# Performance work log

Hardware: AMD Instinct MI355X
Metric: run time of the kernel (lower is better)

The kernel has to match this reference:

```python
import jax, jax.numpy as jnp
import numpy as np

B, N, D, E = 128, 512, 256, 8192  # graphs, nodes/graph, embed_dim, edges/graph
K = int(np.ceil(0.8 * N))         # TopKPooling ratio=0.8 -> k per graph


def setup_inputs() -> dict:
    key = jax.random.key(0)
    ks = jax.random.split(key, 16)
    Ntot = B * N
    x = jax.random.normal(ks[0], (Ntot, 4), jnp.float32)
    offs = (jnp.arange(B, dtype=jnp.int32) * N)[:, None]
    src = (jax.random.randint(ks[1], (B, E), 0, N, jnp.int32) + offs).reshape(-1)
    dst = (jax.random.randint(ks[2], (B, E), 0, N, jnp.int32) + offs).reshape(-1)
    s = 0.05
    w = lambda k, shape: jax.random.normal(k, shape, jnp.float32) * s
    return {
        'x': x, 'src': src, 'dst': dst,
        'Wr1': w(ks[3], (4, D)), 'Ws1': w(ks[4], (4, D)), 'b1': jnp.zeros((D,), jnp.float32),
        'Wr2': w(ks[5], (D, D)), 'Ws2': w(ks[6], (D, D)), 'b2': jnp.zeros((D,), jnp.float32),
        'Wr3': w(ks[7], (D, D)), 'Ws3': w(ks[8], (D, D)), 'b3': jnp.zeros((D,), jnp.float32),
        'p_attn': w(ks[9], (D,)),
        'W1': w(ks[10], (2 * D, D)), 'c1': jnp.zeros((D,), jnp.float32),
        'W2': w(ks[11], (D, D // 2)), 'c2': jnp.zeros((D // 2,), jnp.float32),
        'W3': w(ks[12], (D // 2, 1)), 'c3': jnp.zeros((1,), jnp.float32),
    }


def _graph_conv(x, src, dst, Wr, Ws, b):
    # PyG GraphConv, aggr='add': out = lin_rel(sum_{j in N(i)} x_j) + lin_root(x_i)
    agg = jax.ops.segment_sum(x[src], dst, num_segments=B * N)
    return agg @ Wr + b + x @ Ws


def _gmp_gap(xb):
    # xb: [B, n, D] -> concat(global max pool, global mean pool): [B, 2D]
    return jnp.concatenate([xb.max(axis=1), xb.mean(axis=1)], axis=1)


def reference(x, src, dst, Wr1, Ws1, b1, Wr2, Ws2, b2, Wr3, Ws3, b3,
              p_attn, W1, c1, W2, c2, W3, c3):
    h = jax.nn.relu(_graph_conv(x, src, dst, Wr1, Ws1, b1))
    x1 = _gmp_gap(h.reshape(B, N, D))
    h = jax.nn.relu(_graph_conv(h, src, dst, Wr2, Ws2, b2))
    x2 = _gmp_gap(h.reshape(B, N, D))
    h = jax.nn.relu(_graph_conv(h, src, dst, Wr3, Ws3, b3))
    # TopKPooling: score = x.p/||p||; keep top-k per graph; scale by tanh(score)
    score = (h @ p_attn) / (jnp.linalg.norm(p_attn) + 1e-16)
    vals, idx = jax.lax.top_k(score.reshape(B, N), K)           # [B, K]
    hb = h.reshape(B, N, D)
    sel = jnp.take_along_axis(hb, idx[:, :, None], axis=1) * jnp.tanh(vals)[:, :, None]
    x3 = _gmp_gap(sel)
    z = x1 + x2 + x3
    z = jax.nn.relu(z @ W1 + c1)
    z = jax.nn.relu(z @ W2 + c2)  # dropout is identity in eval mode
    return jax.nn.sigmoid(z @ W3 + c3)[:, 0]
```

## Files before the change

kernel.cpp:

```cpp
#include <hip/hip_runtime.h>

typedef unsigned short u16;
typedef unsigned int u32;

#define B_GRAPHS 128
#define N_NODES  512
#define D_DIM    256
#define E_EDGES  8192
#define K_TOP    410
#define CSR_STRIDE 12288
#define AS 132

typedef __attribute__((ext_vector_type(8))) __bf16 bf16x8;
typedef __attribute__((ext_vector_type(4))) float  f32x4;

__device__ __forceinline__ float bf2f(u16 h) {
  union { u32 u; float f; } c; c.u = ((u32)h) << 16; return c.f;
}
__device__ __forceinline__ float u2f(u32 u) {
  union { u32 u; float f; } c; c.u = u; return c.f;
}
__device__ __forceinline__ u16 f2bf(float f) {
  union { float f; u32 u; } c; c.f = f;
  u32 u = c.u;
  u += 0x7fffu + ((u >> 16) & 1u);
  return (u16)(u >> 16);
}
__device__ __forceinline__ void async_copy16(const void* g, void* l) {
  __builtin_amdgcn_global_load_lds((const __attribute__((address_space(1))) void*)g,
                                   (__attribute__((address_space(3))) void*)l, 16, 0, 0);
}

__global__ void zero_kernel(float* __restrict__ p) {
  *(float4*)&p[(size_t)(blockIdx.x * 256 + threadIdx.x) * 4] = float4{0.f, 0.f, 0.f, 0.f};
}

__global__ void prep_kernel(const float* __restrict__ Wr2, const float* __restrict__ Ws2,
                            const float* __restrict__ Wr3, const float* __restrict__ Ws3,
                            u16* __restrict__ WT) {
  const int mat = blockIdx.y;
  const int n = blockIdx.x;
  const int k = threadIdx.x;
  const float* W = (mat == 0) ? Wr2 : (mat == 1) ? Ws2 : (mat == 2) ? Wr3 : Ws3;
  WT[((size_t)mat << 16) + ((size_t)n << 8) + k] = f2bf(W[(size_t)k * 256 + n]);
}

__global__ __launch_bounds__(256) void csr_kernel(const int* __restrict__ src,
                                                  const int* __restrict__ dst,
                                                  u16* __restrict__ csr_col,
                                                  u32* __restrict__ csr_off) {
  __shared__ u32 cnt[512];
  __shared__ u32 poff[513];
  const int g = blockIdx.x, t = threadIdx.x;
  const int base = g * N_NODES, ebase = g * E_EDGES;
  for (int i = t; i < 512; i += 256) cnt[i] = 0;
  __syncthreads();
  for (int e = t; e < E_EDGES; e += 256)
    atomicAdd(&cnt[dst[ebase + e] - base], 1u);
  __syncthreads();
  if (t == 0) {
    u32 run = 0;
    for (int i = 0; i < 512; ++i) { poff[i] = run; run += (cnt[i] + 7u) & ~7u; }
    poff[512] = run;
  }
  __syncthreads();
  for (int i = t; i < 513; i += 256) csr_off[(size_t)g * 513 + i] = poff[i];
  for (int i = t; i < 512; i += 256) {
    const u32 s = poff[i] + cnt[i], e2 = poff[i + 1];
    for (u32 k = s; k < e2; ++k) csr_col[(size_t)g * CSR_STRIDE + k] = 512;
  }
  __syncthreads();
  for (int i = t; i < 512; i += 256) cnt[i] = poff[i];
  __syncthreads();
  for (int e = t; e < E_EDGES; e += 256) {
    const int d = dst[ebase + e] - base;
    const int s = src[ebase + e] - base;
    const u32 pos = atomicAdd(&cnt[d], 1u);
    csr_col[(size_t)g * CSR_STRIDE + pos] = (u16)s;
  }
}

__global__ __launch_bounds__(256) void conv1_kernel(const float* __restrict__ x,
                             const u16* __restrict__ csr_col, const u32* __restrict__ csr_off,
                             const float* __restrict__ Wr1, const float* __restrict__ Ws1,
                             const float* __restrict__ b1,
                             u16* __restrict__ H1, float* __restrict__ X1) {
  __shared__ float xs[513 * 4];
  __shared__ float aggs[N_NODES * 5];
  __shared__ __align__(16) u16 cols[CSR_STRIDE];
  __shared__ u32 offs[513];
  const int c = blockIdx.x;
  const int g = blockIdx.y;
  const int base = g * N_NODES;
  const int t = threadIdx.x;

  for (int i = t; i < N_NODES; i += 256)
    *(float4*)&xs[i * 4] = *(const float4*)&x[(size_t)(base + i) * 4];
  if (t < 4) xs[512 * 4 + t] = 0.f;
  for (int i = t; i < CSR_STRIDE / 2; i += 256)
    ((u32*)cols)[i] = ((const u32*)(csr_col + (size_t)g * CSR_STRIDE))[i];
  for (int i = t; i < 513; i += 256) offs[i] = csr_off[(size_t)g * 513 + i];
  __syncthreads();

  #pragma unroll
  for (int nn = 0; nn < 2; ++nn) {
    const int i = t * 2 + nn;
    const u32 s0 = offs[i];
    const int nb = (int)((offs[i + 1] - s0) >> 3);
    float a0 = 0.f, a1 = 0.f, a2 = 0.f, a3 = 0.f;
    for (int b = 0; b < nb; ++b) {
      const uint4 cw = *(const uint4*)&cols[s0 + (u32)b * 8];
      const u32 ww[4] = {cw.x, cw.y, cw.z, cw.w};
      #pragma unroll
      for (int q = 0; q < 4; ++q) {
        const int ca = ww[q] & 0xffffu, cb = ww[q] >> 16;
        const float4 va = *(const float4*)&xs[ca * 4];
        const float4 vb = *(const float4*)&xs[cb * 4];
        a0 += va.x + vb.x; a1 += va.y + vb.y;
        a2 += va.z + vb.z; a3 += va.w + vb.w;
      }
    }
    aggs[i * 5 + 0] = a0; aggs[i * 5 + 1] = a1;
    aggs[i * 5 + 2] = a2; aggs[i * 5 + 3] = a3;
  }
  __syncthreads();

  float wr[4], wsv[4];
  #pragma unroll
  for (int k = 0; k < 4; ++k) { wr[k] = Wr1[k * 256 + t]; wsv[k] = Ws1[k * 256 + t]; }
  const float bb = b1[t];
  float mx = 0.f, sm = 0.f;
  const int nlo = c * 256;
  for (int n = nlo; n < nlo + 256; ++n) {
    float acc = bb;
    #pragma unroll
    for (int k = 0; k < 4; ++k) acc += aggs[n * 5 + k] * wr[k] + xs[n * 4 + k] * wsv[k];
    acc = fmaxf(acc, 0.f);
    H1[(size_t)(base + n) * D_DIM + t] = f2bf(acc);
    mx = fmaxf(mx, acc);
    sm += acc;
  }
  atomicMax((int*)&X1[(size_t)g * 512 + t], __float_as_int(mx));
  atomicAdd(&X1[(size_t)g * 512 + 256 + t], sm);
}

__global__ __launch_bounds__(512) void agg_gather_kernel(const u16* __restrict__ H,
                                                         const u16* __restrict__ csr_col,
                                                         const u32* __restrict__ csr_off,
                                                         u16* __restrict__ AGG) {
  __shared__ __align__(16) u16 hs[513 * AS];
  __shared__ __align__(16) u16 cols[CSR_STRIDE];
  __shared__ u32 offs[513];
  const int c = blockIdx.x;
  const int g = blockIdx.y;
  const int base = g * N_NODES;
  const int t = threadIdx.x;

  #pragma unroll
  for (int p = 0; p < 32; ++p) {
    const int flat = p * 512 + t;
    const int row = flat >> 5, q = flat & 31;
    *(uint2*)&hs[row * AS + q * 4] =
        *(const uint2*)&H[(size_t)(base + row) * D_DIM + c * 128 + q * 4];
  }
  if (t < 33) *(uint2*)&hs[512 * AS + t * 4] = uint2{0u, 0u};
  #pragma unroll
  for (int p = 0; p < 12; ++p)
    ((u32*)cols)[p * 512 + t] = ((const u32*)(csr_col + (size_t)g * CSR_STRIDE))[p * 512 + t];
  for (int i = t; i < 513; i += 512) offs[i] = csr_off[(size_t)g * 513 + i];
  __syncthreads();

  const int w = t >> 6, lane = t & 63;
  const int h2 = lane >> 5, fl = lane & 31;
  const int i0 = w * 64;
  for (int i = i0; i < i0 + 64; ++i) {
    const u32 s0 = offs[i];
    const int nb = (int)((offs[i + 1] - s0) >> 3);
    float a0 = 0.f, a1 = 0.f, a2 = 0.f, a3 = 0.f;
    if (nb > 0) {
      uint4 cw = *(const uint4*)&cols[s0];
      for (int b = 0; b < nb; ++b) {
        uint4 cwn = cw;
        if (b + 1 < nb) cwn = *(const uint4*)&cols[s0 + (u32)(b + 1) * 8];
        const u32 w01 = h2 ? cw.z : cw.x;
        const u32 w23 = h2 ? cw.w : cw.y;
        const int c0 = w01 & 0xffffu, c1 = w01 >> 16;
        const int c2 = w23 & 0xffffu, c3 = w23 >> 16;
        const uint2 d0 = *(const uint2*)&hs[c0 * AS + fl * 4];
        const uint2 d1 = *(const uint2*)&hs[c1 * AS + fl * 4];
        const uint2 d2 = *(const uint2*)&hs[c2 * AS + fl * 4];
        const uint2 d3 = *(const uint2*)&hs[c3 * AS + fl * 4];
        a0 += u2f(d0.x << 16); a1 += u2f(d0.x & 0xffff0000u);
        a2 += u2f(d0.y << 16); a3 += u2f(d0.y & 0xffff0000u);
        a0 += u2f(d1.x << 16); a1 += u2f(d1.x & 0xffff0000u);
        a2 += u2f(d1.y << 16); a3 += u2f(d1.y & 0xffff0000u);
        a0 += u2f(d2.x << 16); a1 += u2f(d2.x & 0xffff0000u);
        a2 += u2f(d2.y << 16); a3 += u2f(d2.y & 0xffff0000u);
        a0 += u2f(d3.x << 16); a1 += u2f(d3.x & 0xffff0000u);
        a2 += u2f(d3.y << 16); a3 += u2f(d3.y & 0xffff0000u);
        cw = cwn;
      }
    }
    a0 += __shfl_xor(a0, 32); a1 += __shfl_xor(a1, 32);
    a2 += __shfl_xor(a2, 32); a3 += __shfl_xor(a3, 32);
    if (h2 == 0) {
      uint2 o;
      o.x = (u32)f2bf(a0) | ((u32)f2bf(a1) << 16);
      o.y = (u32)f2bf(a2) | ((u32)f2bf(a3) << 16);
      *(uint2*)&AGG[(size_t)(base + i) * D_DIM + c * 128 + fl * 4] = o;
    }
  }
}

__global__ __launch_bounds__(256) void gemm_kernel(const u16* __restrict__ Amat,
                                                   const u16* __restrict__ Hmat,
                                                   const u16* __restrict__ WrT,
                                                   const u16* __restrict__ WsT,
                                                   const float* __restrict__ bias,
                                                   u16* __restrict__ Hout,
                                                   float* __restrict__ x2pool,
                                                   float* __restrict__ score,
                                                   const float* __restrict__ pvec) {
  __shared__ __align__(16) u16 At[128 * 32];
  __shared__ __align__(16) u16 Bt[128 * 32];
  const int m0 = blockIdx.x * 128;
  const int n0 = blockIdx.y * 128;
  const int t = threadIdx.x;
  const int wid = t >> 6, lane = t & 63;
  const int wm = wid >> 1, wn = wid & 1;
  const int r16 = lane & 15, q0 = lane >> 4;

  f32x4 acc[4][4];
  const f32x4 zero = {0.f, 0.f, 0.f, 0.f};
  #pragma unroll
  for (int i = 0; i < 4; ++i)
    #pragma unroll
    for (int jj = 0; jj < 4; ++jj) acc[i][jj] = zero;

  const int srow_off = lane >> 2;
  const int sq = lane & 3;

  #pragma unroll 1
  for (int s = 0; s < 16; ++s) {
    const int ph = s >> 3;
    const int kk = (s & 7) * 32;
    const u16* Ain = ph ? Hmat : Amat;
    const u16* Win = ph ? WsT : WrT;
    #pragma unroll
    for (int j = 0; j < 4; ++j) {
      const int chk = wid * 4 + j;
      const int ch8 = chk & 7;
      const int r = ch8 * 16 + srow_off;
      const int qsrc = sq ^ ((r >> 1) & 3);
      if (chk < 8)
        async_copy16(&Ain[(size_t)(m0 + r) * 256 + kk + qsrc * 8], &At[ch8 * 512]);
      else
        async_copy16(&Win[(size_t)(n0 + r) * 256 + kk + qsrc * 8], &Bt[ch8 * 512]);
    }
    asm volatile("s_waitcnt vmcnt(0)" ::: "memory");
    __syncthreads();
    bf16x8 aF[4], bF[4];
    #pragma unroll
    for (int mi = 0; mi < 4; ++mi) {
      const int arow = wm * 64 + mi * 16 + r16;
      const int qs = q0 ^ ((arow >> 1) & 3);
      aF[mi] = *(const bf16x8*)&At[arow * 32 + qs * 8];
    }
    #pragma unroll
    for (int ni = 0; ni < 4; ++ni) {
      const int brow = wn * 64 + ni * 16 + r16;
      const int qs = q0 ^ ((brow >> 1) & 3);
      bF[ni] = *(const bf16x8*)&Bt[brow * 32 + qs * 8];
    }
    #pragma unroll
    for (int mi = 0; mi < 4; ++mi)
      #pragma unroll
      for (int ni = 0; ni < 4; ++ni)
        acc[mi][ni] = __builtin_amdgcn_mfma_f32_16x16x32_bf16(aF[mi], bF[ni],
                                                              acc[mi][ni], 0, 0, 0);
    __syncthreads();
  }

  const bool do_x2 = (x2pool != nullptr);
  const bool do_sc = (score != nullptr);
  float colmax[4], colsum[4], pv[4], rpart[4][4];
  #pragma unroll
  for (int ni = 0; ni < 4; ++ni) { colmax[ni] = 0.f; colsum[ni] = 0.f; pv[ni] = 0.f; }
  #pragma unroll
  for (int mi = 0; mi < 4; ++mi)
    #pragma unroll
    for (int r = 0; r < 4; ++r) rpart[mi][r] = 0.f;
  if (do_sc) {
    #pragma unroll
    for (int ni = 0; ni < 4; ++ni) pv[ni] = pvec[n0 + wn * 64 + ni * 16 + r16];
  }

  #pragma unroll
  for (int mi = 0; mi < 4; ++mi) {
    const int growb = m0 + wm * 64 + mi * 16 + q0 * 4;
    #pragma unroll
    for (int ni = 0; ni < 4; ++ni) {
      const int gcol = n0 + wn * 64 + ni * 16 + r16;
      const float bv = bias[gcol];
      #pragma unroll
      for (int r = 0; r < 4; ++r) {
        float v = acc[mi][ni][r] + bv;
        v = fmaxf(v, 0.f);
        Hout[(size_t)(growb + r) * 256 + gcol] = f2bf(v);
        colmax[ni] = fmaxf(colmax[ni], v);
        colsum[ni] += v;
        rpart[mi][r] += v * pv[ni];
      }
    }
  }

  const int gg = m0 >> 9;
  if (do_x2) {
    #pragma unroll
    for (int ni = 0; ni < 4; ++ni) {
      const int gcol = n0 + wn * 64 + ni * 16 + r16;
      float cm = colmax[ni], cs = colsum[ni];
      cm = fmaxf(cm, __shfl_xor(cm, 16));
      cm = fmaxf(cm, __shfl_xor(cm, 32));
      cs += __shfl_xor(cs, 16);
      cs += __shfl_xor(cs, 32);
      if (q0 == 0) {
        atomicMax((int*)&x2pool[(size_t)gg * 512 + gcol], __float_as_int(cm));
        atomicAdd(&x2pool[(size_t)gg * 512 + 256 + gcol], cs);
      }
    }
  }
  if (do_sc) {
    #pragma unroll
    for (int mi = 0; mi < 4; ++mi) {
      const int growb = m0 + wm * 64 + mi * 16 + q0 * 4;
      #pragma unroll
      for (int r = 0; r < 4; ++r) {
        float sp = rpart[mi][r];
        sp += __shfl_xor(sp, 1);
        sp += __shfl_xor(sp, 2);
        sp += __shfl_xor(sp, 4);
        sp += __shfl_xor(sp, 8);
        if (r16 == 0) atomicAdd(&score[growb + r], sp);
      }
    }
  }
}

__global__ __launch_bounds__(256) void sort_kernel(const float* __restrict__ score,
                                                   const float* __restrict__ p,
                                                   u16* __restrict__ top_idx,
                                                   float* __restrict__ top_scale) {
  __shared__ float sval[N_NODES];
  __shared__ int sidx[N_NODES];
  __shared__ float wsum[4];
  const int g = blockIdx.x, t = threadIdx.x;

  float pvt = p[t];
  float sq2 = pvt * pvt;
  #pragma unroll
  for (int off = 32; off > 0; off >>= 1) sq2 += __shfl_down(sq2, off);
  if ((t & 63) == 0) wsum[t >> 6] = sq2;
  __syncthreads();
  const float inv_pn = 1.f / (sqrtf(wsum[0] + wsum[1] + wsum[2] + wsum[3]) + 1e-16f);

  for (int n = t; n < N_NODES; n += 256) {
    sval[n] = score[(size_t)g * 512 + n] * inv_pn;
    sidx[n] = n;
  }
  __syncthreads();

  for (int k = 2; k <= N_NODES; k <<= 1) {
    for (int jj = k >> 1; jj > 0; jj >>= 1) {
      const int i = ((t & ~(jj - 1)) << 1) | (t & (jj - 1));
      const int ix = i | jj;
      const bool dirDesc = ((i & k) == 0);
      const float vi = sval[i], vx = sval[ix];
      const int ii = sidx[i], ij = sidx[ix];
      const bool iAfter = (vi < vx) || (vi == vx && ii > ij);
      if (dirDesc ? iAfter : !iAfter) {
        sval[i] = vx; sval[ix] = vi;
        sidx[i] = ij; sidx[ix] = ii;
      }
      __syncthreads();
    }
  }

  for (int s = t; s < K_TOP; s += 256) {
    top_idx[(size_t)g * 416 + s] = (u16)sidx[s];
    top_scale[(size_t)g * 416 + s] = tanhf(sval[s]);
  }
}

__global__ __launch_bounds__(256) void x3_pool_kernel(const u16* __restrict__ H3,
                                                      const u16* __restrict__ top_idx,
                                                      const float* __restrict__ top_scale,
                                                      float* __restrict__ X3) {
  __shared__ u16 sidxL[416];
  __shared__ float ssclL[416];
  __shared__ float redm[32 * 65];
  __shared__ float reds[32 * 65];
  const int c = blockIdx.x;
  const int g = blockIdx.y;
  const int t = threadIdx.x;
  const int fl = t & 7, rg = t >> 3;

  for (int s = t; s < K_TOP; s += 256) {
    sidxL[s] = top_idx[(size_t)g * 416 + s];
    ssclL[s] = top_scale[(size_t)g * 416 + s];
  }
  __syncthreads();

  float mx[8], sm[8];
  #pragma unroll
  for (int j = 0; j < 8; ++j) { mx[j] = -1e30f; sm[j] = 0.f; }
  const size_t rowbase = (size_t)g * 512;
  for (int s = rg; s < K_TOP; s += 32) {
    const int row = sidxL[s];
    const float sc = ssclL[s];
    const uint4 d = *(const uint4*)&H3[(rowbase + row) * 256 + c * 64 + fl * 8];
    const u32 wv[4] = {d.x, d.y, d.z, d.w};
    #pragma unroll
    for (int q = 0; q < 4; ++q) {
      const float v0 = u2f(wv[q] << 16) * sc;
      const float v1 = u2f(wv[q] & 0xffff0000u) * sc;
      mx[q * 2] = fmaxf(mx[q * 2], v0); sm[q * 2] += v0;
      mx[q * 2 + 1] = fmaxf(mx[q * 2 + 1], v1); sm[q * 2 + 1] += v1;
    }
  }
  #pragma unroll
  for (int j = 0; j < 8; ++j) {
    redm[rg * 65 + fl * 8 + j] = mx[j];
    reds[rg * 65 + fl * 8 + j] = sm[j];
  }
  __syncthreads();
  for (int st = 16; st >= 1; st >>= 1) {
    if (rg < st) {
      #pragma unroll
      for (int j = 0; j < 8; ++j) {
        const int a = rg * 65 + fl * 8 + j, b = (rg + st) * 65 + fl * 8 + j;
        redm[a] = fmaxf(redm[a], redm[b]);
        reds[a] += reds[b];
      }
    }
    __syncthreads();
  }
  if (rg == 0) {
    #pragma unroll
    for (int j = 0; j < 8; ++j) {
      X3[(size_t)g * 512 + c * 64 + fl * 8 + j] = redm[fl * 8 + j];
      X3[(size_t)g * 512 + 256 + c * 64 + fl * 8 + j] = reds[fl * 8 + j] * (1.f / (float)K_TOP);
    }
  }
}

__global__ void mlp_kernel(const float* __restrict__ X1, const float* __restrict__ X2,
                           const float* __restrict__ X3,
                           const float* __restrict__ W1, const float* __restrict__ c1,
                           const float* __restrict__ W2, const float* __restrict__ c2,
                           const float* __restrict__ W3, const float* __restrict__ c3,
                           float* __restrict__ out) {
  __shared__ float zs[512];
  __shared__ float z1[256];
  __shared__ float z2[128];
  const int g = blockIdx.x, t = threadIdx.x;
  for (int k = t; k < 512; k += 256) {
    const float x1v = X1[(size_t)g * 512 + k];
    const float x2v = X2[(size_t)g * 512 + k];
    const float x3v = X3[(size_t)g * 512 + k];
    zs[k] = (k < 256) ? (x1v + x2v + x3v)
                      : (x1v * (1.f / 512.f) + x2v * (1.f / 512.f) + x3v);
  }
  __syncthreads();
  {
    float acc = c1[t];
    for (int k = 0; k < 512; ++k) acc += zs[k] * W1[(size_t)k * 256 + t];
    z1[t] = fmaxf(acc, 0.f);
  }
  __syncthreads();
  if (t < 128) {
    float acc = c2[t];
    for (int d = 0; d < 256; ++d) acc += z1[d] * W2[(size_t)d * 128 + t];
    z2[t] = fmaxf(acc, 0.f);
  }
  __syncthreads();
  if (t == 0) {
    float acc = c3[0];
    for (int e = 0; e < 128; ++e) acc += z2[e] * W3[e];
    out[g] = 1.f / (1.f + expf(-acc));
  }
}

extern "C" void kernel_launch(void* const* d_in, const int* in_sizes, int n_in,
                              void* d_out, int out_size, void* d_ws, size_t ws_size,
                              hipStream_t stream) {
  (void)in_sizes; (void)n_in; (void)out_size; (void)ws_size;
  const float* x   = (const float*)d_in[0];
  const int* src   = (const int*)d_in[1];
  const int* dstp  = (const int*)d_in[2];
  const float* Wr1 = (const float*)d_in[3];
  const float* Ws1 = (const float*)d_in[4];
  const float* b1  = (const float*)d_in[5];
  const float* Wr2 = (const float*)d_in[6];
  const float* Ws2 = (const float*)d_in[7];
  const float* b2  = (const float*)d_in[8];
  const float* Wr3 = (const float*)d_in[9];
  const float* Ws3 = (const float*)d_in[10];
  const float* b3  = (const float*)d_in[11];
  const float* pat = (const float*)d_in[12];
  const float* W1  = (const float*)d_in[13];
  const float* c1  = (const float*)d_in[14];
  const float* W2  = (const float*)d_in[15];
  const float* c2  = (const float*)d_in[16];
  const float* W3  = (const float*)d_in[17];
  const float* c3  = (const float*)d_in[18];
  float* out = (float*)d_out;

  char* ws = (char*)d_ws;
  u16* hA  = (u16*)(ws);
  u16* hB  = (u16*)(ws + 33554432);
  u16* AGG = (u16*)(ws + 67108864);
  u16* WT  = (u16*)(ws + 100663296);
  float* x1 = (float*)(ws + 101187584);
  float* x2 = (float*)(ws + 101449728);
  float* x3 = (float*)(ws + 101711872);
  u16* csr_col = (u16*)(ws + 101974016);
  u32* csr_off = (u32*)(ws + 105119744);
  float* score     = (float*)(ws + 101974016);
  u16* top_idx     = (u16*)(ws + 101974016 + 262144);
  float* top_scale = (float*)(ws + 101974016 + 372736);

  prep_kernel<<<dim3(256, 4), dim3(256), 0, stream>>>(Wr2, Ws2, Wr3, Ws3, WT);
  csr_kernel<<<dim3(128), dim3(256), 0, stream>>>(src, dstp, csr_col, csr_off);
  zero_kernel<<<dim3(128), dim3(256), 0, stream>>>(x1);
  conv1_kernel<<<dim3(2, 128), dim3(256), 0, stream>>>(x, csr_col, csr_off, Wr1, Ws1, b1, hA, x1);

  agg_gather_kernel<<<dim3(2, 128), dim3(512), 0, stream>>>(hA, csr_col, csr_off, AGG);
  gemm_kernel<<<dim3(512, 2), dim3(256), 0, stream>>>(AGG, hA, WT, WT + 65536, b2, hB,
                                                      x2, nullptr, nullptr);

  agg_gather_kernel<<<dim3(2, 128), dim3(512), 0, stream>>>(hB, csr_col, csr_off, AGG);
  zero_kernel<<<dim3(64), dim3(256), 0, stream>>>(score);
  gemm_kernel<<<dim3(512, 2), dim3(256), 0, stream>>>(AGG, hB, WT + 131072, WT + 196608, b3, hA,
                                                      nullptr, score, pat);

  sort_kernel<<<dim3(128), dim3(256), 0, stream>>>(score, pat, top_idx, top_scale);
  x3_pool_kernel<<<dim3(4, 128), dim3(256), 0, stream>>>(hA, top_idx, top_scale, x3);
  mlp_kernel<<<dim3(128), dim3(256), 0, stream>>>(x1, x2, x3, W1, c1, W2, c2, W3, c3, out);
}
```

Baseline: 283.5 us.

## Double-buffer GEMM loads, interleave gather rows, parallelize CSR prefix scan

```diff
diff --git a/kernel.cpp b/kernel.cpp
--- a/kernel.cpp
+++ b/kernel.cpp
@@ -50,6 +50,7 @@
                                                   u16* __restrict__ csr_col,
                                                   u32* __restrict__ csr_off) {
   __shared__ u32 cnt[512];
+  __shared__ u32 scan[512];
   __shared__ u32 poff[513];
   const int g = blockIdx.x, t = threadIdx.x;
   const int base = g * N_NODES, ebase = g * E_EDGES;
@@ -58,11 +59,19 @@
   for (int e = t; e < E_EDGES; e += 256)
     atomicAdd(&cnt[dst[ebase + e] - base], 1u);
   __syncthreads();
-  if (t == 0) {
-    u32 run = 0;
-    for (int i = 0; i < 512; ++i) { poff[i] = run; run += (cnt[i] + 7u) & ~7u; }
-    poff[512] = run;
-  }
+  for (int i = t; i < 512; i += 256) scan[i] = (cnt[i] + 7u) & ~7u;
+  __syncthreads();
+  #pragma unroll 1
+  for (int d = 1; d < 512; d <<= 1) {
+    const u32 v0 = (t >= d) ? scan[t - d] : 0u;
+    const u32 v1 = scan[t + 256 - d];
+    __syncthreads();
+    if (t >= d) scan[t] += v0;
+    scan[t + 256] += v1;
+    __syncthreads();
+  }
+  if (t == 0) poff[0] = 0;
+  for (int i = t; i < 512; i += 256) poff[i + 1] = scan[i];
   __syncthreads();
   for (int i = t; i < 513; i += 256) csr_off[(size_t)g * 513 + i] = poff[i];
   for (int i = t; i < 512; i += 256) {
@@ -149,7 +158,7 @@
                                                          const u32* __restrict__ csr_off,
                                                          u16* __restrict__ AGG) {
   __shared__ __align__(16) u16 hs[513 * AS];
-  __shared__ __align__(16) u16 cols[CSR_STRIDE];
+  __shared__ __align__(16) u16 cols[CSR_STRIDE + 8];
   __shared__ u32 offs[513];
   const int c = blockIdx.x;
   const int g = blockIdx.y;
@@ -167,47 +176,60 @@
   #pragma unroll
   for (int p = 0; p < 12; ++p)
     ((u32*)cols)[p * 512 + t] = ((const u32*)(csr_col + (size_t)g * CSR_STRIDE))[p * 512 + t];
+  if (t < 8) cols[CSR_STRIDE + t] = 512;
   for (int i = t; i < 513; i += 512) offs[i] = csr_off[(size_t)g * 513 + i];
   __syncthreads();
 
   const int w = t >> 6, lane = t & 63;
   const int h2 = lane >> 5, fl = lane & 31;
   const int i0 = w * 64;
-  for (int i = i0; i < i0 + 64; ++i) {
-    const u32 s0 = offs[i];
-    const int nb = (int)((offs[i + 1] - s0) >> 3);
-    float a0 = 0.f, a1 = 0.f, a2 = 0.f, a3 = 0.f;
-    if (nb > 0) {
-      uint4 cw = *(const uint4*)&cols[s0];
-      for (int b = 0; b < nb; ++b) {
-        uint4 cwn = cw;
-        if (b + 1 < nb) cwn = *(const uint4*)&cols[s0 + (u32)(b + 1) * 8];
+  #pragma unroll 1
+  for (int j = 0; j < 16; ++j) {
+    u32 s0[4]; int nb[4];
+    #pragma unroll
+    for (int q = 0; q < 4; ++q) {
+      const int r = i0 + q * 16 + j;
+      s0[q] = offs[r];
+      nb[q] = (int)((offs[r + 1] - s0[q]) >> 3);
+    }
+    const int nbmax = max(max(nb[0], nb[1]), max(nb[2], nb[3]));
+    float a[4][4];
+    #pragma unroll
+    for (int q = 0; q < 4; ++q) { a[q][0] = 0.f; a[q][1] = 0.f; a[q][2] = 0.f; a[q][3] = 0.f; }
+    #pragma unroll 1
+    for (int b = 0; b < nbmax; ++b) {
+      #pragma unroll
+      for (int q = 0; q < 4; ++q) {
+        const u32 ca = (b < nb[q]) ? (s0[q] + (u32)b * 8u) : (u32)CSR_STRIDE;
+        const uint4 cw = *(const uint4*)&cols[ca];
         const u32 w01 = h2 ? cw.z : cw.x;
         const u32 w23 = h2 ? cw.w : cw.y;
-        const int c0 = w01 & 0xffffu, c1 = w01 >> 16;
-        const int c2 = w23 & 0xffffu, c3 = w23 >> 16;
+        const int c0 = (int)(w01 & 0xffffu), c1 = (int)(w01 >> 16);
+        const int c2 = (int)(w23 & 0xffffu), c3 = (int)(w23 >> 16);
         const uint2 d0 = *(const uint2*)&hs[c0 * AS + fl * 4];
         const uint2 d1 = *(const uint2*)&hs[c1 * AS + fl * 4];
         const uint2 d2 = *(const uint2*)&hs[c2 * AS + fl * 4];
         const uint2 d3 = *(const uint2*)&hs[c3 * AS + fl * 4];
-        a0 += u2f(d0.x << 16); a1 += u2f(d0.x & 0xffff0000u);
-        a2 += u2f(d0.y << 16); a3 += u2f(d0.y & 0xffff0000u);
-        a0 += u2f(d1.x << 16); a1 += u2f(d1.x & 0xffff0000u);
-        a2 += u2f(d1.y << 16); a3 += u2f(d1.y & 0xffff0000u);
-        a0 += u2f(d2.x << 16); a1 += u2f(d2.x & 0xffff0000u);
-        a2 += u2f(d2.y << 16); a3 += u2f(d2.y & 0xffff0000u);
-        a0 += u2f(d3.x << 16); a1 += u2f(d3.x & 0xffff0000u);
-        a2 += u2f(d3.y << 16); a3 += u2f(d3.y & 0xffff0000u);
-        cw = cwn;
-      }
-    }
-    a0 += __shfl_xor(a0, 32); a1 += __shfl_xor(a1, 32);
-    a2 += __shfl_xor(a2, 32); a3 += __shfl_xor(a3, 32);
-    if (h2 == 0) {
-      uint2 o;
-      o.x = (u32)f2bf(a0) | ((u32)f2bf(a1) << 16);
-      o.y = (u32)f2bf(a2) | ((u32)f2bf(a3) << 16);
-      *(uint2*)&AGG[(size_t)(base + i) * D_DIM + c * 128 + fl * 4] = o;
+        a[q][0] += (u2f(d0.x << 16) + u2f(d1.x << 16)) + (u2f(d2.x << 16) + u2f(d3.x << 16));
+        a[q][1] += (u2f(d0.x & 0xffff0000u) + u2f(d1.x & 0xffff0000u))
+                 + (u2f(d2.x & 0xffff0000u) + u2f(d3.x & 0xffff0000u));
+        a[q][2] += (u2f(d0.y << 16) + u2f(d1.y << 16)) + (u2f(d2.y << 16) + u2f(d3.y << 16));
+        a[q][3] += (u2f(d0.y & 0xffff0000u) + u2f(d1.y & 0xffff0000u))
+                 + (u2f(d2.y & 0xffff0000u) + u2f(d3.y & 0xffff0000u));
+      }
+    }
+    #pragma unroll
+    for (int q = 0; q < 4; ++q) {
+      const float r0 = a[q][0] + __shfl_xor(a[q][0], 32);
+      const float r1 = a[q][1] + __shfl_xor(a[q][1], 32);
+      const float r2 = a[q][2] + __shfl_xor(a[q][2], 32);
+      const float r3 = a[q][3] + __shfl_xor(a[q][3], 32);
+      if (h2 == 0) {
+        uint2 o;
+        o.x = (u32)f2bf(r0) | ((u32)f2bf(r1) << 16);
+        o.y = (u32)f2bf(r2) | ((u32)f2bf(r3) << 16);
+        *(uint2*)&AGG[(size_t)(base + i0 + q * 16 + j) * D_DIM + c * 128 + fl * 4] = o;
+      }
     }
   }
 }
@@ -221,8 +243,8 @@
                                                    float* __restrict__ x2pool,
                                                    float* __restrict__ score,
                                                    const float* __restrict__ pvec) {
-  __shared__ __align__(16) u16 At[128 * 32];
-  __shared__ __align__(16) u16 Bt[128 * 32];
+  __shared__ __align__(16) u16 At[2][128 * 32];
+  __shared__ __align__(16) u16 Bt[2][128 * 32];
   const int m0 = blockIdx.x * 128;
   const int n0 = blockIdx.y * 128;
   const int t = threadIdx.x;
@@ -240,8 +262,8 @@
   const int srow_off = lane >> 2;
   const int sq = lane & 3;
 
-  #pragma unroll 1
-  for (int s = 0; s < 16; ++s) {
+  auto stage = [&](int s) {
+    const int buf = s & 1;
     const int ph = s >> 3;
     const int kk = (s & 7) * 32;
     const u16* Ain = ph ? Hmat : Amat;
@@ -253,24 +275,35 @@
       const int r = ch8 * 16 + srow_off;
       const int qsrc = sq ^ ((r >> 1) & 3);
       if (chk < 8)
-        async_copy16(&Ain[(size_t)(m0 + r) * 256 + kk + qsrc * 8], &At[ch8 * 512]);
+        async_copy16(&Ain[(size_t)(m0 + r) * 256 + kk + qsrc * 8], &At[buf][ch8 * 512]);
       else
-        async_copy16(&Win[(size_t)(n0 + r) * 256 + kk + qsrc * 8], &Bt[ch8 * 512]);
-    }
-    asm volatile("s_waitcnt vmcnt(0)" ::: "memory");
-    __syncthreads();
+        async_copy16(&Win[(size_t)(n0 + r) * 256 + kk + qsrc * 8], &Bt[buf][ch8 * 512]);
+    }
+  };
+
+  stage(0);
+  #pragma unroll 1
+  for (int s = 0; s < 16; ++s) {
+    if (s < 15) {
+      stage(s + 1);
+      asm volatile("s_waitcnt vmcnt(4)" ::: "memory");
+    } else {
+      asm volatile("s_waitcnt vmcnt(0)" ::: "memory");
+    }
+    __builtin_amdgcn_s_barrier();
+    const int buf = s & 1;
     bf16x8 aF[4], bF[4];
     #pragma unroll
     for (int mi = 0; mi < 4; ++mi) {
       const int arow = wm * 64 + mi * 16 + r16;
       const int qs = q0 ^ ((arow >> 1) & 3);
-      aF[mi] = *(const bf16x8*)&At[arow * 32 + qs * 8];
+      aF[mi] = *(const bf16x8*)&At[buf][arow * 32 + qs * 8];
     }
     #pragma unroll
     for (int ni = 0; ni < 4; ++ni) {
       const int brow = wn * 64 + ni * 16 + r16;
       const int qs = q0 ^ ((brow >> 1) & 3);
-      bF[ni] = *(const bf16x8*)&Bt[brow * 32 + qs * 8];
+      bF[ni] = *(const bf16x8*)&Bt[buf][brow * 32 + qs * 8];
     }
     #pragma unroll
     for (int mi = 0; mi < 4; ++mi)
@@ -278,7 +311,7 @@
       for (int ni = 0; ni < 4; ++ni)
         acc[mi][ni] = __builtin_amdgcn_mfma_f32_16x16x32_bf16(aF[mi], bF[ni],
                                                               acc[mi][ni], 0, 0, 0);
-    __syncthreads();
+    __builtin_amdgcn_s_barrier();
   }
 
   const bool do_x2 = (x2pool != nullptr);
```

Result: faster. 267.1 us (-5.8%).
